# Kernel optimization log

Hardware: AMD Instinct MI355X
Metric: run time of the kernel (lower is better)

Reference implementation:

```python
import jax, jax.numpy as jnp
import numpy as np

H = 64          # HIDDEN_DIM
V = 64          # VOCAB_SIZE
THR = 0.4       # ENERGY_THRESHOLD
LN_EPS = 1e-5
NORM_EPS = 1e-12


def _layer_norm(x, g, b):
    mu = jnp.mean(x, axis=-1, keepdims=True)
    var = jnp.var(x, axis=-1, keepdims=True)
    return (x - mu) * jax.lax.rsqrt(var + LN_EPS) * g + b


def setup_inputs() -> dict:
    key = jax.random.key(0)
    ks = jax.random.split(key, 12)
    B, L = 256, 2048
    s = 0.05
    return {
        "x": jax.random.randint(ks[0], (B, L), 0, V),
        "embed": jax.random.normal(ks[1], (V, H), jnp.float32) * s,
        "w1": jax.random.normal(ks[2], (H, 2 * H), jnp.float32) * s,
        "b1": jnp.zeros((2 * H,), jnp.float32),
        "w2": jax.random.normal(ks[3], (2 * H, H), jnp.float32) * s,
        "b2": jnp.zeros((H,), jnp.float32),
        "ln_g": jnp.ones((H,), jnp.float32),
        "ln_b": jnp.zeros((H,), jnp.float32),
        "wk": jax.random.normal(ks[4], (H, H), jnp.float32) * s,
        "wv": jax.random.normal(ks[5], (H, H), jnp.float32) * s,
        "wq": jax.random.normal(ks[6], (H, H), jnp.float32) * s,
        "wo": jax.random.normal(ks[7], (H, V), jnp.float32) * s,
        "bo": jnp.zeros((V,), jnp.float32),
    }


def reference(x, embed, w1, b1, w2, b2, ln_g, ln_b, wk, wv, wq, wo, bo):
    # Encoder: embed -> FFN -> residual -> LayerNorm
    h = embed[x]                                        # [B, L, H]
    ff = jax.nn.relu(h @ w1 + b1) @ w2 + b2
    h = _layer_norm(h + ff, ln_g, ln_b)                 # [B, L, H]

    B = h.shape[0]
    # Precompute all k (L2-normalized) and v projections, then scan over time.
    k = h @ wk                                          # [B, L, H]
    k = k / jnp.maximum(jnp.linalg.norm(k, axis=-1, keepdims=True), NORM_EPS)
    v = h @ wv                                          # [B, L, H]

    def step(M, kv):
        k_t, v_t = kv                                   # each [B, H]
        pred = jnp.einsum('bij,bj->bi', M, k_t)         # [B, H]
        delta = v_t - pred
        gate = (jnp.linalg.norm(delta, axis=-1, keepdims=True)
                > THR * jnp.linalg.norm(v_t, axis=-1, keepdims=True)).astype(M.dtype)
        M = M + gate[:, :, None] * jnp.einsum('bi,bj->bij', delta, k_t)
        return M, None

    M0 = jnp.zeros((B, H, H), h.dtype)
    M, _ = jax.lax.scan(step, M0,
                        (jnp.swapaxes(k, 0, 1), jnp.swapaxes(v, 0, 1)))

    q = h[:, -1, :] @ wq                                # [B, H]
    read = jax.nn.relu(jnp.einsum('bij,bj->bi', M, q))  # [B, H]
    return read @ wo + bo                               # [B, V]
```

## Files before the change

### kernel.cpp

```cpp
#include <hip/hip_runtime.h>
#include <hip/hip_bf16.h>

#define HD   64
#define SEQ  2048
#define NB   256
#define TWOH 128
#define NCH  32
#define KS   68

typedef float v4f __attribute__((ext_vector_type(4)));

template <int CTRL>
__device__ __forceinline__ float dpp_add(float x) {
    int y = __builtin_amdgcn_update_dpp(0, __builtin_bit_cast(int, x),
                                        CTRL, 0xF, 0xF, true);
    return x + __builtin_bit_cast(float, y);
}

__device__ __forceinline__ float wave_total(float x) {
    x = dpp_add<0x111>(x);
    x = dpp_add<0x112>(x);
    x = dpp_add<0x114>(x);
    x = dpp_add<0x118>(x);
    x = dpp_add<0x142>(x);
    x = dpp_add<0x143>(x);
    return __builtin_bit_cast(float,
        __builtin_amdgcn_readlane(__builtin_bit_cast(int, x), 63));
}

__device__ __forceinline__ float bcastf(float v, int l) {
    return __builtin_bit_cast(float,
        __builtin_amdgcn_readlane(__builtin_bit_cast(int, v), l));
}

__device__ __forceinline__ float hsum4(v4f a) {
    return (a.x + a.y) + (a.z + a.w);
}

__device__ __forceinline__ bool detect_bf16(const void* embed, int lane) {
    const unsigned short* u = (const unsigned short*)embed;
    int bad = 0;
    for (int i = 2 * lane; i < 4096; i += 128) {
        float v = __uint_as_float(((unsigned int)u[i]) << 16);
        if (!(fabsf(v) < 1e4f)) bad = 1;
    }
    return !__any(bad);
}

template <bool BF>
__device__ __forceinline__ float ldf(const void* p, int i) {
    if (BF) return __bfloat162float(((const __hip_bfloat16*)p)[i]);
    return ((const float*)p)[i];
}

template <bool BF>
__device__ void encode_reg(int wid, int lane, int tl, const void* embed,
                           const void* w1, const void* b1, const void* w2,
                           const void* b2, const void* ln_g, const void* ln_b,
                           const void* wk, const void* wvp, const void* wq,
                           float* __restrict__ k_lds, float* __restrict__ v_lds,
                           float* __restrict__ thr2_lds,
                           float* __restrict__ qrow_s) {
    const int tbase = wid * 16;
    float h[16];
    #pragma unroll
    for (int it = 0; it < 16; ++it)
        h[it] = ldf<BF>(embed, (tbase + it) * HD + lane);

    float u0[16], u1[16];
    #pragma unroll
    for (int it = 0; it < 16; ++it) { u0[it] = 0.f; u1[it] = 0.f; }
    float a0 = ldf<BF>(w1, 0 * TWOH + lane), b0 = ldf<BF>(w1, 0 * TWOH + lane + HD);
    float a1 = ldf<BF>(w1, 1 * TWOH + lane), b1w = ldf<BF>(w1, 1 * TWOH + lane + HD);
    float a2 = ldf<BF>(w1, 2 * TWOH + lane), b2w = ldf<BF>(w1, 2 * TWOH + lane + HD);
    float a3 = ldf<BF>(w1, 3 * TWOH + lane), b3w = ldf<BF>(w1, 3 * TWOH + lane + HD);
    #pragma unroll 1
    for (int j4 = 0; j4 < 16; ++j4) {
        float na0 = 0, nb0 = 0, na1 = 0, nb1 = 0,
              na2 = 0, nb2 = 0, na3 = 0, nb3 = 0;
        if (j4 < 15) {
            const int j = (j4 + 1) * 4;
            na0 = ldf<BF>(w1, (j + 0) * TWOH + lane);
            nb0 = ldf<BF>(w1, (j + 0) * TWOH + lane + HD);
            na1 = ldf<BF>(w1, (j + 1) * TWOH + lane);
            nb1 = ldf<BF>(w1, (j + 1) * TWOH + lane + HD);
            na2 = ldf<BF>(w1, (j + 2) * TWOH + lane);
            nb2 = ldf<BF>(w1, (j + 2) * TWOH + lane + HD);
            na3 = ldf<BF>(w1, (j + 3) * TWOH + lane);
            nb3 = ldf<BF>(w1, (j + 3) * TWOH + lane + HD);
        }
        const int j = j4 * 4;
        #pragma unroll
        for (int it = 0; it < 16; ++it) {
            const float s0 = bcastf(h[it], j + 0);
            const float s1 = bcastf(h[it], j + 1);
            const float s2 = bcastf(h[it], j + 2);
            const float s3 = bcastf(h[it], j + 3);
            u0[it] = fmaf(s0, a0, u0[it]); u1[it] = fmaf(s0, b0, u1[it]);
            u0[it] = fmaf(s1, a1, u0[it]); u1[it] = fmaf(s1, b1w, u1[it]);
            u0[it] = fmaf(s2, a2, u0[it]); u1[it] = fmaf(s2, b2w, u1[it]);
            u0[it] = fmaf(s3, a3, u0[it]); u1[it] = fmaf(s3, b3w, u1[it]);
        }
        a0 = na0; b0 = nb0; a1 = na1; b1w = nb1;
        a2 = na2; b2w = nb2; a3 = na3; b3w = nb3;
    }
    const float bb0 = ldf<BF>(b1, lane), bb1 = ldf<BF>(b1, lane + HD);
    #pragma unroll
    for (int it = 0; it < 16; ++it) {
        u0[it] = fmaxf(u0[it] + bb0, 0.f);
        u1[it] = fmaxf(u1[it] + bb1, 0.f);
    }

    float f[16];
    #pragma unroll
    for (int it = 0; it < 16; ++it) f[it] = 0.f;
    {
        float w0 = ldf<BF>(w2, 0 * HD + lane), w1v = ldf<BF>(w2, 1 * HD + lane);
        float w2v = ldf<BF>(w2, 2 * HD + lane), w3 = ldf<BF>(w2, 3 * HD + lane);
        #pragma unroll 1
        for (int e4 = 0; e4 < 16; ++e4) {
            float n0 = 0, n1 = 0, n2 = 0, n3 = 0;
            if (e4 < 15) {
                const int e = (e4 + 1) * 4;
                n0 = ldf<BF>(w2, (e + 0) * HD + lane);
                n1 = ldf<BF>(w2, (e + 1) * HD + lane);
                n2 = ldf<BF>(w2, (e + 2) * HD + lane);
                n3 = ldf<BF>(w2, (e + 3) * HD + lane);
            }
            const int e = e4 * 4;
            #pragma unroll
            for (int it = 0; it < 16; ++it) {
                f[it] = fmaf(bcastf(u0[it], e + 0), w0, f[it]);
                f[it] = fmaf(bcastf(u0[it], e + 1), w1v, f[it]);
                f[it] = fmaf(bcastf(u0[it], e + 2), w2v, f[it]);
                f[it] = fmaf(bcastf(u0[it], e + 3), w3, f[it]);
            }
            w0 = n0; w1v = n1; w2v = n2; w3 = n3;
        }
    }
    {
        float w0 = ldf<BF>(w2, 64 * HD + lane), w1v = ldf<BF>(w2, 65 * HD + lane);
        float w2v = ldf<BF>(w2, 66 * HD + lane), w3 = ldf<BF>(w2, 67 * HD + lane);
        #pragma unroll 1
        for (int e4 = 0; e4 < 16; ++e4) {
            float n0 = 0, n1 = 0, n2 = 0, n3 = 0;
            if (e4 < 15) {
                const int e = HD + (e4 + 1) * 4;
                n0 = ldf<BF>(w2, (e + 0) * HD + lane);
                n1 = ldf<BF>(w2, (e + 1) * HD + lane);
                n2 = ldf<BF>(w2, (e + 2) * HD + lane);
                n3 = ldf<BF>(w2, (e + 3) * HD + lane);
            }
            const int e = e4 * 4;
            #pragma unroll
            for (int it = 0; it < 16; ++it) {
                f[it] = fmaf(bcastf(u1[it], e + 0), w0, f[it]);
                f[it] = fmaf(bcastf(u1[it], e + 1), w1v, f[it]);
                f[it] = fmaf(bcastf(u1[it], e + 2), w2v, f[it]);
                f[it] = fmaf(bcastf(u1[it], e + 3), w3, f[it]);
            }
            w0 = n0; w1v = n1; w2v = n2; w3 = n3;
        }
    }

    const float b2v = ldf<BF>(b2, lane);
    const float lg = ldf<BF>(ln_g, lane), lb = ldf<BF>(ln_b, lane);
    float hn[16];
    #pragma unroll 1
    for (int it = 0; it < 16; ++it) {
        float y = h[it] + f[it] + b2v;
        float mu  = wave_total(y) * 0.015625f;
        float dvv = y - mu;
        float var = wave_total(dvv * dvv) * 0.015625f;
        hn[it] = fmaf(dvv * (1.f / sqrtf(var + 1e-5f)), lg, lb);
    }

    float k[16], v[16];
    #pragma unroll
    for (int it = 0; it < 16; ++it) { k[it] = 0.f; v[it] = 0.f; }
    float ka = ldf<BF>(wk, 0 * HD + lane), kb = ldf<BF>(wk, 1 * HD + lane);
    float kc = ldf<BF>(wk, 2 * HD + lane), kd = ldf<BF>(wk, 3 * HD + lane);
    float va = ldf<BF>(wvp, 0 * HD + lane), vb = ldf<BF>(wvp, 1 * HD + lane);
    float vc = ldf<BF>(wvp, 2 * HD + lane), vd = ldf<BF>(wvp, 3 * HD + lane);
    #pragma unroll 1
    for (int j4 = 0; j4 < 16; ++j4) {
        float nka = 0, nkb = 0, nkc = 0, nkd = 0,
              nva = 0, nvb = 0, nvc = 0, nvd = 0;
        if (j4 < 15) {
            const int j = (j4 + 1) * 4;
            nka = ldf<BF>(wk, (j + 0) * HD + lane);
            nkb = ldf<BF>(wk, (j + 1) * HD + lane);
            nkc = ldf<BF>(wk, (j + 2) * HD + lane);
            nkd = ldf<BF>(wk, (j + 3) * HD + lane);
            nva = ldf<BF>(wvp, (j + 0) * HD + lane);
            nvb = ldf<BF>(wvp, (j + 1) * HD + lane);
            nvc = ldf<BF>(wvp, (j + 2) * HD + lane);
            nvd = ldf<BF>(wvp, (j + 3) * HD + lane);
        }
        const int j = j4 * 4;
        #pragma unroll
        for (int it = 0; it < 16; ++it) {
            const float s0 = bcastf(hn[it], j + 0);
            const float s1 = bcastf(hn[it], j + 1);
            const float s2 = bcastf(hn[it], j + 2);
            const float s3 = bcastf(hn[it], j + 3);
            k[it] = fmaf(s0, ka, k[it]); v[it] = fmaf(s0, va, v[it]);
            k[it] = fmaf(s1, kb, k[it]); v[it] = fmaf(s1, vb, v[it]);
            k[it] = fmaf(s2, kc, k[it]); v[it] = fmaf(s2, vc, v[it]);
            k[it] = fmaf(s3, kd, k[it]); v[it] = fmaf(s3, vd, v[it]);
        }
        ka = nka; kb = nkb; kc = nkc; kd = nkd;
        va = nva; vb = nvb; vc = nvc; vd = nvd;
    }

    #pragma unroll 1
    for (int it = 0; it < 16; ++it) {
        const int t = tbase + it;
        float nk = sqrtf(wave_total(k[it] * k[it]));
        float kn = k[it] / fmaxf(nk, 1e-12f);
        float nv2 = wave_total(v[it] * v[it]);
        k_lds[t * KS + lane] = kn;
        v_lds[t * KS + lane] = v[it];
        if (lane == 0) thr2_lds[t] = 0.16f * nv2;
    }

    if (tl >= tbase && tl < tbase + 16) {
        const int it = tl - tbase;
        float q = 0.f;
        #pragma unroll
        for (int j4 = 0; j4 < 16; ++j4) {
            const int j = j4 * 4;
            q = fmaf(bcastf(hn[it], j + 0), ldf<BF>(wq, (j + 0) * HD + lane), q);
            q = fmaf(bcastf(hn[it], j + 1), ldf<BF>(wq, (j + 1) * HD + lane), q);
            q = fmaf(bcastf(hn[it], j + 2), ldf<BF>(wq, (j + 2) * HD + lane), q);
            q = fmaf(bcastf(hn[it], j + 3), ldf<BF>(wq, (j + 3) * HD + lane), q);
        }
        qrow_s[lane] = q;
    }
}

__global__ __launch_bounds__(256, 1) void fused_kernel(
    const int* __restrict__ x, const void* embed, const void* w1,
    const void* b1, const void* w2, const void* b2, const void* ln_g,
    const void* ln_b, const void* wk, const void* wvp, const void* wq,
    const void* wo, const void* bo, void* __restrict__ out) {
    const int b = blockIdx.x, tid = threadIdx.x;
    const int wid = tid >> 6, lane = tid & 63;
    __shared__ __align__(16) float k_lds[64 * KS];
    __shared__ __align__(16) float v_lds[64 * KS];
    __shared__ __align__(16) float g_lds[4096];
    __shared__ int   tok_lds[SEQ];
    __shared__ float thr2_lds[64];
    __shared__ float qrow_s[64];
    __shared__ float pbuf[2][4][64];
    __shared__ __align__(16) float rd_lds[64];

    const int* xr = x + b * SEQ;
    #pragma unroll
    for (int c = 0; c < 8; ++c) tok_lds[c * 256 + tid] = xr[c * 256 + tid];
    const int tl = xr[SEQ - 1];

    const bool bf = detect_bf16(embed, lane);
    if (bf)
        encode_reg<true>(wid, lane, tl, embed, w1, b1, w2, b2, ln_g, ln_b,
                         wk, wvp, wq, k_lds, v_lds, thr2_lds, qrow_s);
    else
        encode_reg<false>(wid, lane, tl, embed, w1, b1, w2, b2, ln_g, ln_b,
                          wk, wvp, wq, k_lds, v_lds, thr2_lds, qrow_s);
    __syncthreads();

    const float thr2 = thr2_lds[lane];

    v4f kreg[16];
    #pragma unroll
    for (int i = 0; i < 16; ++i)
        kreg[i] = *(const v4f*)&k_lds[lane * KS + i * 4];

    v4f cacc = {0.f, 0.f, 0.f, 0.f};
    #pragma unroll
    for (int i = 0; i < 16; ++i) {
        const v4f qv = *(const v4f*)&qrow_s[i * 4];
        cacc = __builtin_elementwise_fma(qv, kreg[i], cacc);
    }
    const float cq = hsum4(cacc);

    #pragma unroll 1
    for (int t0 = 0; t0 < 16; ++t0) {
        const int t = wid * 16 + t0;
        const float* kt = &k_lds[t * KS];
        v4f a = {0.f, 0.f, 0.f, 0.f};
        #pragma unroll
        for (int i = 0; i < 16; ++i) {
            const v4f kv = *(const v4f*)&kt[i * 4];
            a = __builtin_elementwise_fma(kv, kreg[i], a);
        }
        g_lds[t * HD + lane] = hsum4(a);
    }

    v4f dv[4], R[4];
    v4f acc = {0.f, 0.f, 0.f, 0.f};
    #pragma unroll
    for (int i = 0; i < 4; ++i) {
        dv[i] = *(const v4f*)&v_lds[lane * KS + wid * 16 + i * 4];
        R[i]  = (v4f){0.f, 0.f, 0.f, 0.f};
        acc   = __builtin_elementwise_fma(dv[i], dv[i], acc);
    }
    pbuf[0][wid][lane] = hsum4(acc);
    int pp = 1;
    __syncthreads();
    float nd2 = ((pbuf[0][0][lane] + pbuf[0][1][lane]) +
                 (pbuf[0][2][lane] + pbuf[0][3][lane]));
    unsigned long long fireset = __ballot(nd2 > thr2);

    int chunk = tok_lds[lane];
    #pragma unroll 1
    for (int c = 0; c < NCH; ++c) {
        int nxt = 0;
        if (c + 1 < NCH) nxt = tok_lds[(c + 1) * 64 + lane];
        unsigned long long pend = __ballot((int)((fireset >> chunk) & 1ull));
        while (pend) {
            const int s = __builtin_ctzll(pend);
            const int t = __builtin_amdgcn_readlane(chunk, s);
            const float g   = g_lds[t * HD + lane];
            const float cqt = bcastf(cq, t);
            const v4f gs  = {-g, -g, -g, -g};
            const v4f cqs = {cqt, cqt, cqt, cqt};
            v4f q4 = {0.f, 0.f, 0.f, 0.f};
            #pragma unroll
            for (int i = 0; i < 4; ++i) {
                v4f sve;
                sve.x = bcastf(dv[i].x, t);
                sve.y = bcastf(dv[i].y, t);
                sve.z = bcastf(dv[i].z, t);
                sve.w = bcastf(dv[i].w, t);
                dv[i] = __builtin_elementwise_fma(gs, sve, dv[i]);
                R[i]  = __builtin_elementwise_fma(cqs, sve, R[i]);
                q4    = __builtin_elementwise_fma(dv[i], dv[i], q4);
            }
            pbuf[pp][wid][lane] = hsum4(q4);
            __syncthreads();
            nd2 = ((pbuf[pp][0][lane] + pbuf[pp][1][lane]) +
                   (pbuf[pp][2][lane] + pbuf[pp][3][lane]));
            pp ^= 1;
            fireset = __ballot(nd2 > thr2);
            const unsigned long long above =
                (s >= 63) ? 0ull : (~0ull << (s + 1));
            pend = __ballot((int)((fireset >> chunk) & 1ull)) & above;
        }
        chunk = nxt;
    }

    if (lane == 0) {
        #pragma unroll
        for (int i = 0; i < 4; ++i) {
            v4f r = R[i];
            r.x = fmaxf(r.x, 0.f); r.y = fmaxf(r.y, 0.f);
            r.z = fmaxf(r.z, 0.f); r.w = fmaxf(r.w, 0.f);
            *(v4f*)&rd_lds[wid * 16 + i * 4] = r;
        }
    }
    __syncthreads();

    if (wid == 0) {
        if (bf) {
            float acc2 = __bfloat162float(((const __hip_bfloat16*)bo)[lane]);
            #pragma unroll 8
            for (int j = 0; j < HD; ++j)
                acc2 = fmaf(rd_lds[j],
                    __bfloat162float(((const __hip_bfloat16*)wo)[j * HD + lane]),
                    acc2);
            ((__hip_bfloat16*)out)[b * HD + lane] = __float2bfloat16(acc2);
        } else {
            float acc2 = ((const float*)bo)[lane];
            #pragma unroll 8
            for (int j = 0; j < HD; ++j)
                acc2 = fmaf(rd_lds[j], ((const float*)wo)[j * HD + lane], acc2);
            ((float*)out)[b * HD + lane] = acc2;
        }
    }
}

extern "C" void kernel_launch(void* const* d_in, const int* in_sizes, int n_in,
                              void* d_out, int out_size, void* d_ws, size_t ws_size,
                              hipStream_t stream) {
    const int* x      = (const int*)d_in[0];
    const void* embed = d_in[1];
    const void* w1    = d_in[2];
    const void* b1    = d_in[3];
    const void* w2    = d_in[4];
    const void* b2    = d_in[5];
    const void* ln_g  = d_in[6];
    const void* ln_b  = d_in[7];
    const void* wk    = d_in[8];
    const void* wvp   = d_in[9];
    const void* wq    = d_in[10];
    const void* wo    = d_in[11];
    const void* bo    = d_in[12];

    fused_kernel<<<NB, 256, 0, stream>>>(x, embed, w1, b1, w2, b2, ln_g, ln_b,
                                         wk, wvp, wq, wo, bo, d_out);
}
```

Baseline: 295.5 us.

## Speculatively apply next firing update while waiting on barrier-reduced gate

Inside the serial gated-update loop, each wave now guesses the next firing token (assuming the current fire set minus the just-applied token) and computes its update to dv and R right after the barrier. The barrier-reduced norm is then checked, and the speculative work is either kept or rolled back from saved copies. This aims to hide the dependent-chain latency after each __syncthreads behind useful arithmetic. The cost is extra register pressure (saved dv/R copies), an extra ballot per step, and wasted work whenever the guess is wrong.

```diff
diff --git a/kernel.cpp b/kernel.cpp
--- a/kernel.cpp
+++ b/kernel.cpp
@@ -297,7 +297,7 @@
         g_lds[t * HD + lane] = hsum4(a);
     }
 
-    v4f dv[4], R[4];
+    v4f dv[4], R[4], dv_sv[4], R_sv[4];
     v4f acc = {0.f, 0.f, 0.f, 0.f};
     #pragma unroll
     for (int i = 0; i < 4; ++i) {
@@ -318,34 +318,85 @@
         int nxt = 0;
         if (c + 1 < NCH) nxt = tok_lds[(c + 1) * 64 + lane];
         unsigned long long pend = __ballot((int)((fireset >> chunk) & 1ull));
+        bool applied = false;
+        float q4h_sp = 0.f;
         while (pend) {
             const int s = __builtin_ctzll(pend);
             const int t = __builtin_amdgcn_readlane(chunk, s);
-            const float g   = g_lds[t * HD + lane];
-            const float cqt = bcastf(cq, t);
-            const v4f gs  = {-g, -g, -g, -g};
-            const v4f cqs = {cqt, cqt, cqt, cqt};
-            v4f q4 = {0.f, 0.f, 0.f, 0.f};
-            #pragma unroll
-            for (int i = 0; i < 4; ++i) {
-                v4f sve;
-                sve.x = bcastf(dv[i].x, t);
-                sve.y = bcastf(dv[i].y, t);
-                sve.z = bcastf(dv[i].z, t);
-                sve.w = bcastf(dv[i].w, t);
-                dv[i] = __builtin_elementwise_fma(gs, sve, dv[i]);
-                R[i]  = __builtin_elementwise_fma(cqs, sve, R[i]);
-                q4    = __builtin_elementwise_fma(dv[i], dv[i], q4);
-            }
-            pbuf[pp][wid][lane] = hsum4(q4);
-            __syncthreads();
-            nd2 = ((pbuf[pp][0][lane] + pbuf[pp][1][lane]) +
-                   (pbuf[pp][2][lane] + pbuf[pp][3][lane]));
-            pp ^= 1;
-            fireset = __ballot(nd2 > thr2);
+            float q4h;
+            if (applied) {
+                q4h = q4h_sp;
+            } else {
+                const float g   = g_lds[t * HD + lane];
+                const float cqt = bcastf(cq, t);
+                const v4f gs  = {-g, -g, -g, -g};
+                const v4f cqs = {cqt, cqt, cqt, cqt};
+                v4f q4 = {0.f, 0.f, 0.f, 0.f};
+                #pragma unroll
+                for (int i = 0; i < 4; ++i) {
+                    v4f sve;
+                    sve.x = bcastf(dv[i].x, t);
+                    sve.y = bcastf(dv[i].y, t);
+                    sve.z = bcastf(dv[i].z, t);
+                    sve.w = bcastf(dv[i].w, t);
+                    dv[i] = __builtin_elementwise_fma(gs, sve, dv[i]);
+                    R[i]  = __builtin_elementwise_fma(cqs, sve, R[i]);
+                    q4    = __builtin_elementwise_fma(dv[i], dv[i], q4);
+                }
+                q4h = hsum4(q4);
+            }
+            pbuf[pp][wid][lane] = q4h;
+
             const unsigned long long above =
                 (s >= 63) ? 0ull : (~0ull << (s + 1));
+            const unsigned long long fs_sp = fireset & ~(1ull << t);
+            unsigned long long pend_sp =
+                __ballot((int)((fs_sp >> chunk) & 1ull)) & above;
+
+            __syncthreads();
+            const float p0 = pbuf[pp][0][lane];
+            const float p1 = pbuf[pp][1][lane];
+            const float p2 = pbuf[pp][2][lane];
+            const float p3 = pbuf[pp][3][lane];
+            int  s_sp  = 0;
+            bool did_sp = false;
+            if (pend_sp) {
+                s_sp = __builtin_ctzll(pend_sp);
+                const int t2 = __builtin_amdgcn_readlane(chunk, s_sp);
+                const float g2   = g_lds[t2 * HD + lane];
+                const float cqt2 = bcastf(cq, t2);
+                #pragma unroll
+                for (int i = 0; i < 4; ++i) { dv_sv[i] = dv[i]; R_sv[i] = R[i]; }
+                const v4f gs2  = {-g2, -g2, -g2, -g2};
+                const v4f cqs2 = {cqt2, cqt2, cqt2, cqt2};
+                v4f q4b = {0.f, 0.f, 0.f, 0.f};
+                #pragma unroll
+                for (int i = 0; i < 4; ++i) {
+                    v4f sve;
+                    sve.x = bcastf(dv[i].x, t2);
+                    sve.y = bcastf(dv[i].y, t2);
+                    sve.z = bcastf(dv[i].z, t2);
+                    sve.w = bcastf(dv[i].w, t2);
+                    dv[i] = __builtin_elementwise_fma(gs2, sve, dv[i]);
+                    R[i]  = __builtin_elementwise_fma(cqs2, sve, R[i]);
+                    q4b   = __builtin_elementwise_fma(dv[i], dv[i], q4b);
+                }
+                q4h_sp = hsum4(q4b);
+                did_sp = true;
+            }
+            const float nd2n = (p0 + p1) + (p2 + p3);
+            pp ^= 1;
+            fireset = __ballot(nd2n > thr2);
             pend = __ballot((int)((fireset >> chunk) & 1ull)) & above;
+            if (did_sp && pend != 0ull && __builtin_ctzll(pend) == s_sp) {
+                applied = true;
+            } else {
+                if (did_sp) {
+                    #pragma unroll
+                    for (int i = 0; i < 4; ++i) { dv[i] = dv_sv[i]; R[i] = R_sv[i]; }
+                }
+                applied = false;
+            }
         }
         chunk = nxt;
     }
```

Result: slower. 422.9 us (+43.1%).
